# Performance work log

Hardware: AMD Instinct MI355X
Metric: run time of the kernel (lower is better)

The kernel has to match this reference:

```python
import jax, jax.numpy as jnp
import numpy as np

N_NODES = 100000
N_EDGES = 1600000
IN_DIM, HID_DIM, OUT_DIM = 128, 128, 64


def setup_inputs() -> dict:
    key = jax.random.key(0)
    k1, k2, k3, k4 = jax.random.split(key, 4)
    x = jax.random.normal(k1, (N_NODES, IN_DIM), dtype=jnp.float32)
    edge_index = jax.random.randint(k2, (2, N_EDGES), 0, N_NODES, dtype=jnp.int32)
    # Glorot-ish init for weights
    W1 = jax.random.normal(k3, (IN_DIM, HID_DIM), dtype=jnp.float32) / np.sqrt(IN_DIM)
    W2 = jax.random.normal(k4, (HID_DIM, OUT_DIM), dtype=jnp.float32) / np.sqrt(HID_DIM)
    b1 = jnp.zeros((HID_DIM,), dtype=jnp.float32)
    b2 = jnp.zeros((OUT_DIM,), dtype=jnp.float32)
    return {"x": x, "edge_index": edge_index, "W1": W1, "b1": b1, "W2": W2, "b2": b2}


def _gcn_norm(edge_index, num_nodes):
    # PyG gcn_norm: add self-loops, symmetric normalization deg^-1/2 A deg^-1/2
    loops = jnp.arange(num_nodes, dtype=edge_index.dtype)
    src = jnp.concatenate([edge_index[0], loops])  # [E+N]
    tgt = jnp.concatenate([edge_index[1], loops])
    deg = jax.ops.segment_sum(jnp.ones_like(tgt, dtype=jnp.float32), tgt,
                              num_segments=num_nodes)
    dinv = jnp.where(deg > 0, jax.lax.rsqrt(deg), 0.0)
    norm = dinv[src] * dinv[tgt]  # [E+N]
    return src, tgt, norm


def _gcn_conv(x, W, b, src, tgt, norm, num_nodes):
    h = x @ W                              # [N, D_out] transform first (GCNConv order)
    msg = norm[:, None] * h[src]           # gather + scale per edge
    agg = jax.ops.segment_sum(msg, tgt, num_segments=num_nodes)  # scatter-add
    return agg + b


def reference(x, edge_index, W1, b1, W2, b2):
    n = x.shape[0]
    src, tgt, norm = _gcn_norm(edge_index, n)
    h = jax.nn.relu(_gcn_conv(x, W1, b1, src, tgt, norm, n))
    out = _gcn_conv(h, W2, b2, src, tgt, norm, n)
    return out
```

## Files before the change

kernel.cpp:

```cpp
#include <hip/hip_runtime.h>


typedef unsigned int uint;
typedef unsigned short ushort;
typedef __attribute__((ext_vector_type(8))) short bf16x8;
typedef __attribute__((ext_vector_type(8))) ushort u16x8;
typedef __attribute__((ext_vector_type(4))) float f32x4;

#define BSHIFT 8
#define MAXBK  512
#define NB     256
#define CAP    8192

__device__ inline ushort f2bf(float f) {
    uint u = __float_as_uint(f);
    return (ushort)((u + 0x7fffu + ((u >> 16) & 1u)) >> 16);
}
__device__ inline float bf_lo(uint u) { return __uint_as_float(u << 16); }
__device__ inline float bf_hi(uint u) { return __uint_as_float(u & 0xffff0000u); }

__global__ __launch_bounds__(256) void hist_kernel(const int* __restrict__ tgt,
                                                   int* __restrict__ counts,
                                                   int E, int chunk, int nbk) {
    __shared__ int hist[MAXBK];
    int t = threadIdx.x, b = blockIdx.x;
    for (int i = t; i < nbk; i += 256) hist[i] = 0;
    __syncthreads();
    int s = b * chunk, e = min(E, s + chunk);
    for (int i = s + t; i < e; i += 256) atomicAdd(&hist[tgt[i] >> BSHIFT], 1);
    __syncthreads();
    for (int i = t; i < nbk; i += 256) counts[i * NB + b] = hist[i];
}

__global__ __launch_bounds__(256) void scan_partial(const int* __restrict__ in,
                                                    int* __restrict__ bsum, int M) {
    int t = threadIdx.x, b = blockIdx.x;
    int base = b * 1024 + t * 4;
    int s = 0;
#pragma unroll
    for (int k = 0; k < 4; ++k) s += (base + k < M) ? in[base + k] : 0;
#pragma unroll
    for (int off = 32; off > 0; off >>= 1) s += __shfl_down(s, off, 64);
    __shared__ int ws[4];
    if ((t & 63) == 0) ws[t >> 6] = s;
    __syncthreads();
    if (t == 0) bsum[b] = ws[0] + ws[1] + ws[2] + ws[3];
}

__global__ __launch_bounds__(256) void scan_final_counts(int* __restrict__ counts,
                                                         const int* __restrict__ bsum,
                                                         int M) {
    int t = threadIdx.x, b = blockIdx.x;
    int lane = t & 63, wid = t >> 6;
    int p = 0;
    for (int i = t; i < b; i += 256) p += bsum[i];
#pragma unroll
    for (int off = 32; off > 0; off >>= 1) p += __shfl_down(p, off, 64);
    __shared__ int ps[4];
    if (lane == 0) ps[wid] = p;
    __syncthreads();
    int pre = ps[0] + ps[1] + ps[2] + ps[3];

    int base = b * 1024 + t * 4;
    int d[4];
#pragma unroll
    for (int k = 0; k < 4; ++k) d[k] = (base + k < M) ? counts[base + k] : 0;
    int tot = d[0] + d[1] + d[2] + d[3];
    int incl = tot;
#pragma unroll
    for (int off = 1; off < 64; off <<= 1) {
        int u = __shfl_up(incl, off, 64);
        if (lane >= off) incl += u;
    }
    __shared__ int wsum[4];
    if (lane == 63) wsum[wid] = incl;
    __syncthreads();
    int woff = 0;
    for (int w = 0; w < wid; ++w) woff += wsum[w];
    int run = incl - tot + woff + pre;
#pragma unroll
    for (int k = 0; k < 4; ++k) {
        if (base + k < M) counts[base + k] = run;
        run += d[k];
    }
}

__global__ __launch_bounds__(256) void bucket_scatter(const int* __restrict__ src,
                                                      const int* __restrict__ tgt,
                                                      const int* __restrict__ offsets,
                                                      int* __restrict__ tmpP,
                                                      int E, int chunk, int nbk) {
    __shared__ int cur[MAXBK];
    int t = threadIdx.x, b = blockIdx.x;
    for (int i = t; i < nbk; i += 256) cur[i] = offsets[i * NB + b];
    __syncthreads();
    int s = b * chunk, e = min(E, s + chunk);
    for (int i = s + t; i < e; i += 256) {
        int tg = tgt[i];
        int p = atomicAdd(&cur[tg >> BSHIFT], 1);
        tmpP[p] = (src[i] << BSHIFT) | (tg & 255);
    }
}

__global__ __launch_bounds__(256) void bucket_finish(const int* __restrict__ tmpP,
                                                     const int* __restrict__ offsets,
                                                     int* __restrict__ rowptr,
                                                     float* __restrict__ dinv,
                                                     int* __restrict__ csr_src,
                                                     int N, int E, int nbk) {
    __shared__ int stage[CAP];
    __shared__ int cnt[256];
    __shared__ int wsum[4];
    int t = threadIdx.x, b = blockIdx.x;
    cnt[t] = 0;
    __syncthreads();
    int s = offsets[b * NB];
    int e = (b + 1 < nbk) ? offsets[(b + 1) * NB] : E;
    int m = e - s;
    for (int i = t; i < m; i += 256) {
        int ed = tmpP[s + i];
        if (i < CAP) stage[i] = ed;
        atomicAdd(&cnt[ed & 255], 1);
    }
    __syncthreads();
    int lane = t & 63, wid = t >> 6;
    int d = cnt[t];
    int incl = d;
#pragma unroll
    for (int off = 1; off < 64; off <<= 1) {
        int u = __shfl_up(incl, off, 64);
        if (lane >= off) incl += u;
    }
    if (lane == 63) wsum[wid] = incl;
    __syncthreads();
    int woff = 0;
    for (int w = 0; w < wid; ++w) woff += wsum[w];
    int excl = s + incl - d + woff;
    int node = b * 256 + t;
    if (node < N) {
        rowptr[node] = excl;
        dinv[node] = rsqrtf((float)d + 1.0f);
    }
    if (b == nbk - 1 && t == 255) rowptr[N] = E;
    cnt[t] = excl;
    __syncthreads();
    for (int i = t; i < m; i += 256) {
        int ed = (i < CAP) ? stage[i] : tmpP[s + i];
        int p = atomicAdd(&cnt[ed & 255], 1);
        csr_src[p] = ed >> BSHIFT;
    }
}

template <int M, typename AT>
__global__ __launch_bounds__(256) void gemm_mfma(const AT* __restrict__ A,
                                                 const float* __restrict__ W,
                                                 ushort* __restrict__ C, int N) {
    constexpr int WTS = 136;
    __shared__ ushort WT[M * WTS];
    const int tid = threadIdx.x;
    for (int i = tid; i < 128 * (M / 4); i += 256) {
        int k = i / (M / 4);
        int n0 = (i % (M / 4)) * 4;
        float4 w = *(const float4*)&W[k * M + n0];
        WT[(n0 + 0) * WTS + k] = f2bf(w.x);
        WT[(n0 + 1) * WTS + k] = f2bf(w.y);
        WT[(n0 + 2) * WTS + k] = f2bf(w.z);
        WT[(n0 + 3) * WTS + k] = f2bf(w.w);
    }
    __syncthreads();

    const int wv = tid >> 6, lane = tid & 63;
    const int quad = lane >> 4, mrow = lane & 15;
    int arow_i = blockIdx.x * 64 + wv * 16 + mrow;
    if (arow_i >= N) arow_i = N - 1;
    const AT* arow = &A[(size_t)arow_i * 128];

    f32x4 acc[M / 16];
#pragma unroll
    for (int t = 0; t < M / 16; ++t) acc[t] = (f32x4){0.f, 0.f, 0.f, 0.f};

#pragma unroll
    for (int ks = 0; ks < 4; ++ks) {
        const int k0 = ks * 32 + quad * 8;
        bf16x8 af;
        if constexpr (sizeof(AT) == 4) {
            float4 a0 = *(const float4*)&arow[k0];
            float4 a1 = *(const float4*)&arow[k0 + 4];
            af[0] = (short)f2bf(a0.x); af[1] = (short)f2bf(a0.y);
            af[2] = (short)f2bf(a0.z); af[3] = (short)f2bf(a0.w);
            af[4] = (short)f2bf(a1.x); af[5] = (short)f2bf(a1.y);
            af[6] = (short)f2bf(a1.z); af[7] = (short)f2bf(a1.w);
        } else {
            af = *(const bf16x8*)&arow[k0];
        }
#pragma unroll
        for (int t = 0; t < M / 16; ++t) {
            int n = t * 16 + mrow;
            bf16x8 bfr = *(const bf16x8*)&WT[n * WTS + k0];
            acc[t] = __builtin_amdgcn_mfma_f32_16x16x32_bf16(af, bfr, acc[t], 0, 0, 0);
        }
    }

    const int orow0 = blockIdx.x * 64 + wv * 16 + quad * 4;
#pragma unroll
    for (int r = 0; r < 4; ++r) {
        int orow = orow0 + r;
        if (orow < N) {
#pragma unroll
            for (int t = 0; t < M / 16; ++t)
                C[(size_t)orow * M + t * 16 + mrow] = f2bf(acc[t][r]);
        }
    }
}

template <int D, bool RELU, bool OUTBF>
__global__ __launch_bounds__(256) void gather_kernel(
    const ushort* __restrict__ h, const int* __restrict__ rowptr,
    const int* __restrict__ csr_src, const float* __restrict__ dinv,
    const float* __restrict__ bias, void* __restrict__ outv, int N) {
    constexpr int Q = D / 8;
    constexpr int G = 64 / Q;
    const int wid = threadIdx.x >> 6, lane = threadIdx.x & 63;
    const int node = blockIdx.x * 4 + wid;
    if (node >= N) return;
    const int g = lane / Q, q = lane % Q;
    const int qoff = q * 8;
    const int beg = rowptr[node], end = rowptr[node + 1];
    float acc[8] = {};

    for (int j = beg; j < end; j += 2 * G) {
        int e0 = j + g, e1 = j + G + g;
        {
            bool v = e0 < end;
            int s = v ? csr_src[e0] : node;
            float w = v ? dinv[s] : 0.0f;
            uint4 hv = *(const uint4*)&h[(size_t)s * D + qoff];
            acc[0] += w * bf_lo(hv.x); acc[1] += w * bf_hi(hv.x);
            acc[2] += w * bf_lo(hv.y); acc[3] += w * bf_hi(hv.y);
            acc[4] += w * bf_lo(hv.z); acc[5] += w * bf_hi(hv.z);
            acc[6] += w * bf_lo(hv.w); acc[7] += w * bf_hi(hv.w);
        }
        {
            bool v = e1 < end;
            int s = v ? csr_src[e1] : node;
            float w = v ? dinv[s] : 0.0f;
            uint4 hv = *(const uint4*)&h[(size_t)s * D + qoff];
            acc[0] += w * bf_lo(hv.x); acc[1] += w * bf_hi(hv.x);
            acc[2] += w * bf_lo(hv.y); acc[3] += w * bf_hi(hv.y);
            acc[4] += w * bf_lo(hv.z); acc[5] += w * bf_hi(hv.z);
            acc[6] += w * bf_lo(hv.w); acc[7] += w * bf_hi(hv.w);
        }
    }
#pragma unroll
    for (int m = Q; m < 64; m <<= 1)
#pragma unroll
        for (int k = 0; k < 8; ++k) acc[k] += __shfl_xor(acc[k], m, 64);

    const float di = dinv[node];
    {
        uint4 hv = *(const uint4*)&h[(size_t)node * D + qoff];
        acc[0] += di * bf_lo(hv.x); acc[1] += di * bf_hi(hv.x);
        acc[2] += di * bf_lo(hv.y); acc[3] += di * bf_hi(hv.y);
        acc[4] += di * bf_lo(hv.z); acc[5] += di * bf_hi(hv.z);
        acc[6] += di * bf_lo(hv.w); acc[7] += di * bf_hi(hv.w);
    }
    if (g == 0) {
        float4 b0 = *(const float4*)&bias[qoff];
        float4 b1 = *(const float4*)&bias[qoff + 4];
        float r[8] = {di * acc[0] + b0.x, di * acc[1] + b0.y,
                      di * acc[2] + b0.z, di * acc[3] + b0.w,
                      di * acc[4] + b1.x, di * acc[5] + b1.y,
                      di * acc[6] + b1.z, di * acc[7] + b1.w};
        if (RELU) {
#pragma unroll
            for (int k = 0; k < 8; ++k) r[k] = fmaxf(r[k], 0.0f);
        }
        if constexpr (OUTBF) {
            ushort* out = (ushort*)outv;
            u16x8 o;
#pragma unroll
            for (int k = 0; k < 8; ++k) o[k] = f2bf(r[k]);
            *(u16x8*)&out[(size_t)node * D + qoff] = o;
        } else {
            float* out = (float*)outv;
            *(float4*)&out[(size_t)node * D + qoff]     = make_float4(r[0], r[1], r[2], r[3]);
            *(float4*)&out[(size_t)node * D + qoff + 4] = make_float4(r[4], r[5], r[6], r[7]);
        }
    }
}

extern "C" void kernel_launch(void* const* d_in, const int* in_sizes, int n_in,
                              void* d_out, int out_size, void* d_ws, size_t ws_size,
                              hipStream_t stream) {
    const float* x  = (const float*)d_in[0];
    const int*   ei = (const int*)d_in[1];
    const float* W1 = (const float*)d_in[2];
    const float* b1 = (const float*)d_in[3];
    const float* W2 = (const float*)d_in[4];
    const float* b2 = (const float*)d_in[5];
    float* out = (float*)d_out;

    const int N = in_sizes[0] / 128;
    const int E = in_sizes[1] / 2;
    const int* src = ei;
    const int* tgt = ei + E;

    const int nbk   = (N + 255) >> BSHIFT;
    const int chunk = (E + NB - 1) / NB;
    const int Mc    = nbk * NB;

    float* ws = (float*)d_ws;
    const size_t Np = (size_t)((N + 3) & ~3);
    float*  dinv    = ws;
    int*    rowptr  = (int*)(ws + Np);
    int*    counts  = rowptr + Np + 4;
    int*    bsum    = counts + MAXBK * NB;
    int*    csr_src = bsum + 128;
    int*    tmpP    = csr_src + E;
    ushort* h       = (ushort*)(tmpP + E);
    ushort* h1      = h + (size_t)N * 128;
    ushort* h2      = h;

    const int nbc = (Mc + 1023) / 1024;

    hist_kernel<<<NB, 256, 0, stream>>>(tgt, counts, E, chunk, nbk);
    scan_partial<<<nbc, 256, 0, stream>>>(counts, bsum, Mc);
    scan_final_counts<<<nbc, 256, 0, stream>>>(counts, bsum, Mc);
    bucket_scatter<<<NB, 256, 0, stream>>>(src, tgt, counts, tmpP, E, chunk, nbk);
    bucket_finish<<<nbk, 256, 0, stream>>>(tmpP, counts, rowptr, dinv, csr_src, N, E, nbk);

    gemm_mfma<128, float><<<(N + 63) / 64, 256, 0, stream>>>(x, W1, h, N);
    gather_kernel<128, true, true><<<(N + 3) / 4, 256, 0, stream>>>(
        h, rowptr, csr_src, dinv, b1, h1, N);

    gemm_mfma<64, ushort><<<(N + 63) / 64, 256, 0, stream>>>(h1, W2, h2, N);
    gather_kernel<64, false, false><<<(N + 3) / 4, 256, 0, stream>>>(
        h2, rowptr, csr_src, dinv, b2, out, N);
}
```

Baseline: 324.0 us.

## Split layer-1 features into two 64-wide halves and vectorize bucketing loads

The first GEMM now writes its 128-column output as two separate 64-column bf16 arrays, and the layer-1 aggregation runs as two gather passes of 64 columns each. The aim is to shrink the per-pass gathered working set so it fits better in cache, at the cost of reading the CSR structure twice. The histogram and bucket-scatter kernels also load source and target indices as int4 vectors, with the chunk size rounded up to a multiple of four so those loads stay aligned.

```diff
diff --git a/kernel.cpp b/kernel.cpp
--- a/kernel.cpp
+++ b/kernel.cpp
@@ -27,9 +27,18 @@
     for (int i = t; i < nbk; i += 256) hist[i] = 0;
     __syncthreads();
     int s = b * chunk, e = min(E, s + chunk);
-    for (int i = s + t; i < e; i += 256) atomicAdd(&hist[tgt[i] >> BSHIFT], 1);
-    __syncthreads();
-    for (int i = t; i < nbk; i += 256) counts[i * NB + b] = hist[i];
+    int i = s + t * 4;
+    for (; i + 3 < e; i += 1024) {
+        int4 tv = *(const int4*)&tgt[i];
+        atomicAdd(&hist[tv.x >> BSHIFT], 1);
+        atomicAdd(&hist[tv.y >> BSHIFT], 1);
+        atomicAdd(&hist[tv.z >> BSHIFT], 1);
+        atomicAdd(&hist[tv.w >> BSHIFT], 1);
+    }
+    if (i < e)
+        for (int k = i; k < e; ++k) atomicAdd(&hist[tgt[k] >> BSHIFT], 1);
+    __syncthreads();
+    for (int i2 = t; i2 < nbk; i2 += 256) counts[i2 * NB + b] = hist[i2];
 }
 
 __global__ __launch_bounds__(256) void scan_partial(const int* __restrict__ in,
@@ -95,10 +104,25 @@
     for (int i = t; i < nbk; i += 256) cur[i] = offsets[i * NB + b];
     __syncthreads();
     int s = b * chunk, e = min(E, s + chunk);
-    for (int i = s + t; i < e; i += 256) {
-        int tg = tgt[i];
-        int p = atomicAdd(&cur[tg >> BSHIFT], 1);
-        tmpP[p] = (src[i] << BSHIFT) | (tg & 255);
+    int i = s + t * 4;
+    for (; i + 3 < e; i += 1024) {
+        int4 sv = *(const int4*)&src[i];
+        int4 tv = *(const int4*)&tgt[i];
+        int p0 = atomicAdd(&cur[tv.x >> BSHIFT], 1);
+        tmpP[p0] = (sv.x << BSHIFT) | (tv.x & 255);
+        int p1 = atomicAdd(&cur[tv.y >> BSHIFT], 1);
+        tmpP[p1] = (sv.y << BSHIFT) | (tv.y & 255);
+        int p2 = atomicAdd(&cur[tv.z >> BSHIFT], 1);
+        tmpP[p2] = (sv.z << BSHIFT) | (tv.z & 255);
+        int p3 = atomicAdd(&cur[tv.w >> BSHIFT], 1);
+        tmpP[p3] = (sv.w << BSHIFT) | (tv.w & 255);
+    }
+    if (i < e) {
+        for (int k = i; k < e; ++k) {
+            int tg = tgt[k];
+            int p = atomicAdd(&cur[tg >> BSHIFT], 1);
+            tmpP[p] = (src[k] << BSHIFT) | (tg & 255);
+        }
     }
 }
 
@@ -154,7 +178,8 @@
 template <int M, typename AT>
 __global__ __launch_bounds__(256) void gemm_mfma(const AT* __restrict__ A,
                                                  const float* __restrict__ W,
-                                                 ushort* __restrict__ C, int N) {
+                                                 ushort* __restrict__ C0,
+                                                 ushort* __restrict__ C1, int N) {
     constexpr int WTS = 136;
     __shared__ ushort WT[M * WTS];
     const int tid = threadIdx.x;
@@ -207,34 +232,35 @@
         int orow = orow0 + r;
         if (orow < N) {
 #pragma unroll
-            for (int t = 0; t < M / 16; ++t)
-                C[(size_t)orow * M + t * 16 + mrow] = f2bf(acc[t][r]);
-        }
-    }
-}
-
-template <int D, bool RELU, bool OUTBF>
-__global__ __launch_bounds__(256) void gather_kernel(
+            for (int t = 0; t < M / 16; ++t) {
+                int c = t * 16 + mrow;
+                ushort* Cp = (c < 64) ? C0 : C1;
+                Cp[(size_t)orow * 64 + (c & 63)] = f2bf(acc[t][r]);
+            }
+        }
+    }
+}
+
+template <bool RELU, bool OUTBF, int OS>
+__global__ __launch_bounds__(256) void gather64(
     const ushort* __restrict__ h, const int* __restrict__ rowptr,
     const int* __restrict__ csr_src, const float* __restrict__ dinv,
     const float* __restrict__ bias, void* __restrict__ outv, int N) {
-    constexpr int Q = D / 8;
-    constexpr int G = 64 / Q;
     const int wid = threadIdx.x >> 6, lane = threadIdx.x & 63;
     const int node = blockIdx.x * 4 + wid;
     if (node >= N) return;
-    const int g = lane / Q, q = lane % Q;
+    const int g = lane >> 3, q = lane & 7;
     const int qoff = q * 8;
     const int beg = rowptr[node], end = rowptr[node + 1];
     float acc[8] = {};
 
-    for (int j = beg; j < end; j += 2 * G) {
-        int e0 = j + g, e1 = j + G + g;
+    for (int j = beg; j < end; j += 16) {
+        int e0 = j + g, e1 = j + 8 + g;
         {
             bool v = e0 < end;
             int s = v ? csr_src[e0] : node;
             float w = v ? dinv[s] : 0.0f;
-            uint4 hv = *(const uint4*)&h[(size_t)s * D + qoff];
+            uint4 hv = *(const uint4*)&h[(size_t)s * 64 + qoff];
             acc[0] += w * bf_lo(hv.x); acc[1] += w * bf_hi(hv.x);
             acc[2] += w * bf_lo(hv.y); acc[3] += w * bf_hi(hv.y);
             acc[4] += w * bf_lo(hv.z); acc[5] += w * bf_hi(hv.z);
@@ -244,7 +270,7 @@
             bool v = e1 < end;
             int s = v ? csr_src[e1] : node;
             float w = v ? dinv[s] : 0.0f;
-            uint4 hv = *(const uint4*)&h[(size_t)s * D + qoff];
+            uint4 hv = *(const uint4*)&h[(size_t)s * 64 + qoff];
             acc[0] += w * bf_lo(hv.x); acc[1] += w * bf_hi(hv.x);
             acc[2] += w * bf_lo(hv.y); acc[3] += w * bf_hi(hv.y);
             acc[4] += w * bf_lo(hv.z); acc[5] += w * bf_hi(hv.z);
@@ -252,13 +278,13 @@
         }
     }
 #pragma unroll
-    for (int m = Q; m < 64; m <<= 1)
+    for (int m = 8; m < 64; m <<= 1)
 #pragma unroll
         for (int k = 0; k < 8; ++k) acc[k] += __shfl_xor(acc[k], m, 64);
 
     const float di = dinv[node];
     {
-        uint4 hv = *(const uint4*)&h[(size_t)node * D + qoff];
+        uint4 hv = *(const uint4*)&h[(size_t)node * 64 + qoff];
         acc[0] += di * bf_lo(hv.x); acc[1] += di * bf_hi(hv.x);
         acc[2] += di * bf_lo(hv.y); acc[3] += di * bf_hi(hv.y);
         acc[4] += di * bf_lo(hv.z); acc[5] += di * bf_hi(hv.z);
@@ -280,11 +306,11 @@
             u16x8 o;
 #pragma unroll
             for (int k = 0; k < 8; ++k) o[k] = f2bf(r[k]);
-            *(u16x8*)&out[(size_t)node * D + qoff] = o;
+            *(u16x8*)&out[(size_t)node * OS + qoff] = o;
         } else {
             float* out = (float*)outv;
-            *(float4*)&out[(size_t)node * D + qoff]     = make_float4(r[0], r[1], r[2], r[3]);
-            *(float4*)&out[(size_t)node * D + qoff + 4] = make_float4(r[4], r[5], r[6], r[7]);
+            *(float4*)&out[(size_t)node * OS + qoff]     = make_float4(r[0], r[1], r[2], r[3]);
+            *(float4*)&out[(size_t)node * OS + qoff + 4] = make_float4(r[4], r[5], r[6], r[7]);
         }
     }
 }
@@ -306,7 +332,7 @@
     const int* tgt = ei + E;
 
     const int nbk   = (N + 255) >> BSHIFT;
-    const int chunk = (E + NB - 1) / NB;
+    const int chunk = (((E + NB - 1) / NB) + 3) & ~3;
     const int Mc    = nbk * NB;
 
     float* ws = (float*)d_ws;
@@ -317,9 +343,10 @@
     int*    bsum    = counts + MAXBK * NB;
     int*    csr_src = bsum + 128;
     int*    tmpP    = csr_src + E;
-    ushort* h       = (ushort*)(tmpP + E);
-    ushort* h1      = h + (size_t)N * 128;
-    ushort* h2      = h;
+    ushort* h_a     = (ushort*)(tmpP + E);
+    ushort* h_b     = h_a + (size_t)N * 64;
+    ushort* h1      = h_b + (size_t)N * 64;
+    ushort* h2      = h_a;
 
     const int nbc = (Mc + 1023) / 1024;
 
@@ -329,11 +356,13 @@
     bucket_scatter<<<NB, 256, 0, stream>>>(src, tgt, counts, tmpP, E, chunk, nbk);
     bucket_finish<<<nbk, 256, 0, stream>>>(tmpP, counts, rowptr, dinv, csr_src, N, E, nbk);
 
-    gemm_mfma<128, float><<<(N + 63) / 64, 256, 0, stream>>>(x, W1, h, N);
-    gather_kernel<128, true, true><<<(N + 3) / 4, 256, 0, stream>>>(
-        h, rowptr, csr_src, dinv, b1, h1, N);
-
-    gemm_mfma<64, ushort><<<(N + 63) / 64, 256, 0, stream>>>(h1, W2, h2, N);
-    gather_kernel<64, false, false><<<(N + 3) / 4, 256, 0, stream>>>(
+    gemm_mfma<128, float><<<(N + 63) / 64, 256, 0, stream>>>(x, W1, h_a, h_b, N);
+    gather64<true, true, 128><<<(N + 3) / 4, 256, 0, stream>>>(
+        h_a, rowptr, csr_src, dinv, b1, h1, N);
+    gather64<true, true, 128><<<(N + 3) / 4, 256, 0, stream>>>(
+        h_b, rowptr, csr_src, dinv, b1 + 64, h1 + 64, N);
+
+    gemm_mfma<64, ushort><<<(N + 63) / 64, 256, 0, stream>>>(h1, W2, h2, h2, N);
+    gather64<false, false, 64><<<(N + 3) / 4, 256, 0, stream>>>(
         h2, rowptr, csr_src, dinv, b2, out, N);
 }
```

Result: slower. 336.5 us (+3.8%).

## Fold source-side dinv into GEMM epilogue and vectorize edge-index loads

Applied to the files above, without the earlier changes.

The GEMM epilogue now scales each output row by dinv[row], so the gather kernels no longer need a per-edge dinv[src] lookup. Each edge contributes with unit weight and only the target-side dinv is applied at the end. Separately, the histogram and bucket-scatter kernels read src/tgt as int4 vectors, with the per-block chunk rounded up to a multiple of 4 to keep those loads aligned. This removes one dependent random global load per edge in both aggregation passes, at the cost of an extra bf16 rounding after scaling.

```diff
diff --git a/kernel.cpp b/kernel.cpp
--- a/kernel.cpp
+++ b/kernel.cpp
@@ -27,9 +27,18 @@
     for (int i = t; i < nbk; i += 256) hist[i] = 0;
     __syncthreads();
     int s = b * chunk, e = min(E, s + chunk);
-    for (int i = s + t; i < e; i += 256) atomicAdd(&hist[tgt[i] >> BSHIFT], 1);
-    __syncthreads();
-    for (int i = t; i < nbk; i += 256) counts[i * NB + b] = hist[i];
+    int i = s + t * 4;
+    for (; i + 3 < e; i += 1024) {
+        int4 tv = *(const int4*)&tgt[i];
+        atomicAdd(&hist[tv.x >> BSHIFT], 1);
+        atomicAdd(&hist[tv.y >> BSHIFT], 1);
+        atomicAdd(&hist[tv.z >> BSHIFT], 1);
+        atomicAdd(&hist[tv.w >> BSHIFT], 1);
+    }
+    if (i < e)
+        for (int k = i; k < e; ++k) atomicAdd(&hist[tgt[k] >> BSHIFT], 1);
+    __syncthreads();
+    for (int i2 = t; i2 < nbk; i2 += 256) counts[i2 * NB + b] = hist[i2];
 }
 
 __global__ __launch_bounds__(256) void scan_partial(const int* __restrict__ in,
@@ -95,10 +104,25 @@
     for (int i = t; i < nbk; i += 256) cur[i] = offsets[i * NB + b];
     __syncthreads();
     int s = b * chunk, e = min(E, s + chunk);
-    for (int i = s + t; i < e; i += 256) {
-        int tg = tgt[i];
-        int p = atomicAdd(&cur[tg >> BSHIFT], 1);
-        tmpP[p] = (src[i] << BSHIFT) | (tg & 255);
+    int i = s + t * 4;
+    for (; i + 3 < e; i += 1024) {
+        int4 sv = *(const int4*)&src[i];
+        int4 tv = *(const int4*)&tgt[i];
+        int p0 = atomicAdd(&cur[tv.x >> BSHIFT], 1);
+        tmpP[p0] = (sv.x << BSHIFT) | (tv.x & 255);
+        int p1 = atomicAdd(&cur[tv.y >> BSHIFT], 1);
+        tmpP[p1] = (sv.y << BSHIFT) | (tv.y & 255);
+        int p2 = atomicAdd(&cur[tv.z >> BSHIFT], 1);
+        tmpP[p2] = (sv.z << BSHIFT) | (tv.z & 255);
+        int p3 = atomicAdd(&cur[tv.w >> BSHIFT], 1);
+        tmpP[p3] = (sv.w << BSHIFT) | (tv.w & 255);
+    }
+    if (i < e) {
+        for (int k = i; k < e; ++k) {
+            int tg = tgt[k];
+            int p = atomicAdd(&cur[tg >> BSHIFT], 1);
+            tmpP[p] = (src[k] << BSHIFT) | (tg & 255);
+        }
     }
 }
 
@@ -154,6 +178,7 @@
 template <int M, typename AT>
 __global__ __launch_bounds__(256) void gemm_mfma(const AT* __restrict__ A,
                                                  const float* __restrict__ W,
+                                                 const float* __restrict__ dinv,
                                                  ushort* __restrict__ C, int N) {
     constexpr int WTS = 136;
     __shared__ ushort WT[M * WTS];
@@ -206,9 +231,10 @@
     for (int r = 0; r < 4; ++r) {
         int orow = orow0 + r;
         if (orow < N) {
+            float dv = dinv[orow];
 #pragma unroll
             for (int t = 0; t < M / 16; ++t)
-                C[(size_t)orow * M + t * 16 + mrow] = f2bf(acc[t][r]);
+                C[(size_t)orow * M + t * 16 + mrow] = f2bf(dv * acc[t][r]);
         }
     }
 }
@@ -233,38 +259,38 @@
         {
             bool v = e0 < end;
             int s = v ? csr_src[e0] : node;
-            float w = v ? dinv[s] : 0.0f;
+            float m = v ? 1.0f : 0.0f;
             uint4 hv = *(const uint4*)&h[(size_t)s * D + qoff];
-            acc[0] += w * bf_lo(hv.x); acc[1] += w * bf_hi(hv.x);
-            acc[2] += w * bf_lo(hv.y); acc[3] += w * bf_hi(hv.y);
-            acc[4] += w * bf_lo(hv.z); acc[5] += w * bf_hi(hv.z);
-            acc[6] += w * bf_lo(hv.w); acc[7] += w * bf_hi(hv.w);
+            acc[0] += m * bf_lo(hv.x); acc[1] += m * bf_hi(hv.x);
+            acc[2] += m * bf_lo(hv.y); acc[3] += m * bf_hi(hv.y);
+            acc[4] += m * bf_lo(hv.z); acc[5] += m * bf_hi(hv.z);
+            acc[6] += m * bf_lo(hv.w); acc[7] += m * bf_hi(hv.w);
         }
         {
             bool v = e1 < end;
             int s = v ? csr_src[e1] : node;
-            float w = v ? dinv[s] : 0.0f;
+            float m = v ? 1.0f : 0.0f;
             uint4 hv = *(const uint4*)&h[(size_t)s * D + qoff];
-            acc[0] += w * bf_lo(hv.x); acc[1] += w * bf_hi(hv.x);
-            acc[2] += w * bf_lo(hv.y); acc[3] += w * bf_hi(hv.y);
-            acc[4] += w * bf_lo(hv.z); acc[5] += w * bf_hi(hv.z);
-            acc[6] += w * bf_lo(hv.w); acc[7] += w * bf_hi(hv.w);
-        }
-    }
-#pragma unroll
-    for (int m = Q; m < 64; m <<= 1)
-#pragma unroll
-        for (int k = 0; k < 8; ++k) acc[k] += __shfl_xor(acc[k], m, 64);
-
-    const float di = dinv[node];
+            acc[0] += m * bf_lo(hv.x); acc[1] += m * bf_hi(hv.x);
+            acc[2] += m * bf_lo(hv.y); acc[3] += m * bf_hi(hv.y);
+            acc[4] += m * bf_lo(hv.z); acc[5] += m * bf_hi(hv.z);
+            acc[6] += m * bf_lo(hv.w); acc[7] += m * bf_hi(hv.w);
+        }
+    }
+#pragma unroll
+    for (int m2 = Q; m2 < 64; m2 <<= 1)
+#pragma unroll
+        for (int k = 0; k < 8; ++k) acc[k] += __shfl_xor(acc[k], m2, 64);
+
     {
         uint4 hv = *(const uint4*)&h[(size_t)node * D + qoff];
-        acc[0] += di * bf_lo(hv.x); acc[1] += di * bf_hi(hv.x);
-        acc[2] += di * bf_lo(hv.y); acc[3] += di * bf_hi(hv.y);
-        acc[4] += di * bf_lo(hv.z); acc[5] += di * bf_hi(hv.z);
-        acc[6] += di * bf_lo(hv.w); acc[7] += di * bf_hi(hv.w);
+        acc[0] += bf_lo(hv.x); acc[1] += bf_hi(hv.x);
+        acc[2] += bf_lo(hv.y); acc[3] += bf_hi(hv.y);
+        acc[4] += bf_lo(hv.z); acc[5] += bf_hi(hv.z);
+        acc[6] += bf_lo(hv.w); acc[7] += bf_hi(hv.w);
     }
     if (g == 0) {
+        const float di = dinv[node];
         float4 b0 = *(const float4*)&bias[qoff];
         float4 b1 = *(const float4*)&bias[qoff + 4];
         float r[8] = {di * acc[0] + b0.x, di * acc[1] + b0.y,
@@ -306,7 +332,7 @@
     const int* tgt = ei + E;
 
     const int nbk   = (N + 255) >> BSHIFT;
-    const int chunk = (E + NB - 1) / NB;
+    const int chunk = (((E + NB - 1) / NB) + 3) & ~3;
     const int Mc    = nbk * NB;
 
     float* ws = (float*)d_ws;
@@ -329,11 +355,11 @@
     bucket_scatter<<<NB, 256, 0, stream>>>(src, tgt, counts, tmpP, E, chunk, nbk);
     bucket_finish<<<nbk, 256, 0, stream>>>(tmpP, counts, rowptr, dinv, csr_src, N, E, nbk);
 
-    gemm_mfma<128, float><<<(N + 63) / 64, 256, 0, stream>>>(x, W1, h, N);
+    gemm_mfma<128, float><<<(N + 63) / 64, 256, 0, stream>>>(x, W1, dinv, h, N);
     gather_kernel<128, true, true><<<(N + 3) / 4, 256, 0, stream>>>(
         h, rowptr, csr_src, dinv, b1, h1, N);
 
-    gemm_mfma<64, ushort><<<(N + 63) / 64, 256, 0, stream>>>(h1, W2, h2, N);
+    gemm_mfma<64, ushort><<<(N + 63) / 64, 256, 0, stream>>>(h1, W2, dinv, h2, N);
     gather_kernel<64, false, false><<<(N + 3) / 4, 256, 0, stream>>>(
         h2, rowptr, csr_src, dinv, b2, out, N);
 }
```

Result: faster. 310.5 us (-4.2%).
